# Kernel tuning notes

Hardware: AMD Instinct MI355X
Metric: run time of the kernel (lower is better)

## Reference

```python
import jax, jax.numpy as jnp
import numpy as np

DEGREES = (0, 1, 2, 3)
REPEATS = np.array([2 * l + 1 for l in DEGREES])          # [1,3,5,7]
EV_DIM = int(REPEATS.sum())                               # 16
SEG = np.concatenate([[0], np.cumsum(REPEATS)])
F, H, L = 128, 8, len(DEGREES)
DH, DE = F // H, F // L                                   # 16, 32
NRB, N, E = 32, 16384, 262144
ATT_NORM_INV = float(np.sqrt(DH))
ATT_NORM_EV = float(np.sqrt(DE))


def l0_contraction(ev):
    # per-degree sum of squares over the m components: [..., EV_DIM] -> [..., L]
    return jnp.stack([jnp.sum(ev[..., SEG[i]:SEG[i + 1]] ** 2, axis=-1) for i in range(L)], axis=-1)


def silu(x):
    return x * jax.nn.sigmoid(x)


def filter_net(rbf, ev_inv, w1r, b1r, w2r, b2r, w1e, b1e, w2e, b2e):
    # FilterNet(num_layers=2): Linear+SiLU then Linear+Identity on each branch, summed.
    r = silu(rbf @ w1r + b1r) @ w2r + b2r
    e = silu(ev_inv @ w1e + b1e) @ w2e + b2e
    return r + e


def setup_inputs() -> dict:
    key = jax.random.key(0)
    ks = iter(jax.random.split(key, 40))
    nrm = lambda shape, s=1.0: jax.random.normal(next(ks), shape, dtype=jnp.float32) * s
    s = 0.05
    inp = {
        'inv_features': nrm((N, F)),
        'ev_features': nrm((N, EV_DIM)),
        'rbf': jax.random.uniform(next(ks), (E, NRB), dtype=jnp.float32),
        'sh_vectors': nrm((E, EV_DIM)),
        'cutoffs': jax.random.uniform(next(ks), (E, 1), dtype=jnp.float32),
        'senders': jax.random.randint(next(ks), (E,), 0, N),
        'receivers': jax.random.randint(next(ks), (E,), 0, N),
    }
    for p in ('fi', 'fe'):
        inp[p + '_rbf_w1'] = nrm((NRB, F), s); inp[p + '_rbf_b1'] = jnp.zeros((F,), jnp.float32)
        inp[p + '_rbf_w2'] = nrm((F, F), s);   inp[p + '_rbf_b2'] = jnp.zeros((F,), jnp.float32)
        inp[p + '_ev_w1'] = nrm((L, F // 4), s); inp[p + '_ev_b1'] = jnp.zeros((F // 4,), jnp.float32)
        inp[p + '_ev_w2'] = nrm((F // 4, F), s); inp[p + '_ev_b2'] = jnp.zeros((F,), jnp.float32)
    inp['Wq_inv'] = nrm((H, DH, DH), s)
    inp['Wk_inv'] = nrm((H, DH, DH), s)
    inp['Wv_inv'] = nrm((H, DH, DH), s)
    inp['Wq_ev'] = nrm((L, DE, DE), s)
    inp['Wk_ev'] = nrm((L, DE, DE), s)
    inp['int_w'] = nrm((F + L, F + L), s)
    inp['int_b'] = jnp.zeros((F + L,), jnp.float32)
    return inp


def reference(inv_features, ev_features, rbf, sh_vectors, cutoffs,
              fi_rbf_w1, fi_rbf_b1, fi_rbf_w2, fi_rbf_b2, fi_ev_w1, fi_ev_b1, fi_ev_w2, fi_ev_b2,
              fe_rbf_w1, fe_rbf_b1, fe_rbf_w2, fe_rbf_b2, fe_ev_w1, fe_ev_b1, fe_ev_w2, fe_ev_b2,
              Wq_inv, Wk_inv, Wv_inv, Wq_ev, Wk_ev, int_w, int_b,
              senders, receivers):
    n_nodes = inv_features.shape[0]
    # --- EuclideanAttentionBlock ---
    ev_diff = ev_features[senders] - ev_features[receivers]           # [E, EV_DIM]
    ev_diff_inv = l0_contraction(ev_diff)                             # [E, L]
    fw_inv = filter_net(rbf, ev_diff_inv, fi_rbf_w1, fi_rbf_b1, fi_rbf_w2, fi_rbf_b2,
                        fi_ev_w1, fi_ev_b1, fi_ev_w2, fi_ev_b2).reshape(-1, H, DH)
    fw_ev = filter_net(rbf, ev_diff_inv, fe_rbf_w1, fe_rbf_b1, fe_rbf_w2, fe_rbf_b2,
                       fe_ev_w1, fe_ev_b1, fe_ev_w2, fe_ev_b2).reshape(-1, L, DE)
    x_inv = inv_features.reshape(-1, H, DH)
    x_ev = inv_features.reshape(-1, L, DE)
    # qk_non_linearity = identity (None default)
    q_inv = jnp.einsum('nhd,hde->nhe', x_inv, Wq_inv)[receivers]      # [E, H, DH]
    k_inv = jnp.einsum('nhd,hde->nhe', x_inv, Wk_inv)[senders]
    v_inv = jnp.einsum('nhd,hde->nhe', x_inv, Wv_inv)[senders]
    q_ev = jnp.einsum('nld,lde->nle', x_ev, Wq_ev)[receivers]         # [E, L, DE]
    k_ev = jnp.einsum('nld,lde->nle', x_ev, Wk_ev)[senders]
    alpha_inv = jnp.sum(q_inv * (k_inv * fw_inv), axis=-1, keepdims=True) / ATT_NORM_INV  # [E,H,1]
    alpha_ev = jnp.sum(q_ev * (k_ev * fw_ev), axis=-1) / ATT_NORM_EV                      # [E,L]
    scaled_inv = cutoffs[:, :, None] * alpha_inv * v_inv              # [E, H, DH]
    d_att_inv = jax.ops.segment_sum(scaled_inv, receivers, num_segments=n_nodes).reshape(-1, F)
    alpha_ev_full = jnp.repeat(alpha_ev, REPEATS, axis=-1, total_repeat_length=EV_DIM)    # [E, EV_DIM]
    scaled_ev = cutoffs * alpha_ev_full * sh_vectors
    d_att_ev = jax.ops.segment_sum(scaled_ev, receivers, num_segments=n_nodes)
    inv1 = inv_features + d_att_inv
    ev1 = ev_features + d_att_ev
    # --- InteractionBlock ---
    ev_inv = l0_contraction(ev1)                                      # [N, L]
    t = jnp.concatenate([inv1, ev_inv], axis=-1) @ int_w + int_b      # [N, F+L]
    d_inv2 = t[..., :F]
    b_ev = jnp.repeat(t[..., F:], REPEATS, axis=-1, total_repeat_length=EV_DIM)
    d_ev2 = b_ev * ev1
    return inv1 + d_inv2, ev1 + d_ev2
```

## Files before the change

### kernel.cpp

```cpp
#include <hip/hip_runtime.h>
#include <math.h>

#define NN 16384
#define NRB 32
#define EE 262144
#define TEB 64
#define TPB_E 16

typedef __attribute__((ext_vector_type(8))) short short8v;
typedef __attribute__((ext_vector_type(4))) float f32x4;

__device__ __forceinline__ float silu_f(float x) {
    return x * __builtin_amdgcn_rcpf(1.0f + __expf(-x));
}
__device__ __forceinline__ int degmap(int j) { return (j == 0) ? 0 : (j < 4) ? 1 : (j < 9) ? 2 : 3; }
__device__ __forceinline__ unsigned short f2b(float f) {
    unsigned int u = __float_as_uint(f);
    unsigned int r = (u + 0x7FFFu + ((u >> 16) & 1u)) >> 16;
    return (unsigned short)r;
}
__device__ __forceinline__ unsigned short f2bt(float f) {
    return (unsigned short)(__float_as_uint(f) >> 16);
}
__device__ __forceinline__ float b2f(short s) {
    return __uint_as_float(((unsigned int)(unsigned short)s) << 16);
}

__global__ __launch_bounds__(256) void fused_prep(
    const float* __restrict__ fi_w1r, const float* __restrict__ fi_w2r,
    const float* __restrict__ fi_w2e,
    const float* __restrict__ fe_w1r, const float* __restrict__ fe_w2r,
    const float* __restrict__ fe_w2e,
    unsigned short* __restrict__ wbf,
    const int* __restrict__ recv,
    int* __restrict__ cnt)
{
    const int tid = threadIdx.x;
    if (blockIdx.x < 192) {
        const int id = blockIdx.x * 256 + tid;
        if (id >= 2 * 24576) return;
        const int p = id / 24576;
        const int r = id % 24576;
        const float* w1r = p ? fe_w1r : fi_w1r;
        const float* w2r = p ? fe_w2r : fi_w2r;
        const float* w2e = p ? fe_w2e : fi_w2e;
        float v;
        if (r < 4096) {
            v = w1r[(r & 31) * 128 + (r >> 5)];
        } else if (r < 20480) {
            const int rr = r - 4096;
            v = w2r[(rr & 127) * 128 + (rr >> 7)];
        } else {
            const int rr = r - 20480;
            v = w2e[(rr & 31) * 128 + (rr >> 5)];
        }
        wbf[p * 24576 + r] = f2b(v);
    } else {
        const int e = (blockIdx.x - 192) * 256 + tid;
        if (e < EE) atomicAdd(&cnt[recv[e]], 1);
    }
}

__global__ __launch_bounds__(256) void csr_scan(const int* __restrict__ cnt,
                                                int* __restrict__ off) {
    __shared__ int ps[256];
    const int t = threadIdx.x;
    const int base = t * 64;
    int s = 0;
    for (int i = 0; i < 64; ++i) s += cnt[base + i];
    ps[t] = s;
    __syncthreads();
    for (int dd = 1; dd < 256; dd <<= 1) {
        int v = 0;
        if (t >= dd) v = ps[t - dd];
        __syncthreads();
        ps[t] += v;
        __syncthreads();
    }
    int run = ps[t] - s;
    for (int i = 0; i < 64; ++i) {
        off[base + i] = run;
        run += cnt[base + i];
    }
}

__global__ __launch_bounds__(256) void fused_fill(
    const int* __restrict__ recv,
    const int* __restrict__ send,
    const float* __restrict__ rbf,
    const float* __restrict__ cutoffs,
    const float* __restrict__ ev_feat,
    const float* __restrict__ sh,
    const int* __restrict__ off,
    int* __restrict__ cursor,
    int* __restrict__ s_sid,
    int* __restrict__ s_rid,
    unsigned short* __restrict__ rbf_s,
    float* __restrict__ cut_s,
    float* __restrict__ evinv_s,
    unsigned short* __restrict__ sh_s,
    const float* __restrict__ inv,
    const float* __restrict__ Wq_inv, const float* __restrict__ Wk_inv,
    const float* __restrict__ Wv_inv,
    const float* __restrict__ Wq_ev, const float* __restrict__ Wk_ev,
    unsigned short* __restrict__ q_inv, unsigned short* __restrict__ k_inv,
    unsigned short* __restrict__ v_inv,
    unsigned short* __restrict__ q_ev, unsigned short* __restrict__ k_ev)
{
    const int tid = threadIdx.x;
    if (blockIdx.x < 1024) {
        const int e = blockIdx.x * 256 + tid;
        if (e < EE) {
            const int r = recv[e];
            const int s = send[e];
            const int p = off[r] + atomicAdd(&cursor[r], 1);
            s_sid[p] = s;
            s_rid[p] = r;
            cut_s[p] = cutoffs[e];
            const float* src = rbf + (size_t)e * 32;
            unsigned short* dst = rbf_s + (size_t)p * 32;
            #pragma unroll
            for (int c = 0; c < 4; ++c) {
                const float4 a = *(const float4*)(src + c * 8);
                const float4 b = *(const float4*)(src + c * 8 + 4);
                short8v pk;
                pk[0] = f2b(a.x); pk[1] = f2b(a.y); pk[2] = f2b(a.z); pk[3] = f2b(a.w);
                pk[4] = f2b(b.x); pk[5] = f2b(b.y); pk[6] = f2b(b.z); pk[7] = f2b(b.w);
                *(short8v*)(dst + c * 8) = pk;
            }
            const float* shp = sh + (size_t)e * 16;
            unsigned short* shd = sh_s + (size_t)p * 16;
            #pragma unroll
            for (int c = 0; c < 2; ++c) {
                const float4 a = *(const float4*)(shp + c * 8);
                const float4 b = *(const float4*)(shp + c * 8 + 4);
                short8v pk;
                pk[0] = f2b(a.x); pk[1] = f2b(a.y); pk[2] = f2b(a.z); pk[3] = f2b(a.w);
                pk[4] = f2b(b.x); pk[5] = f2b(b.y); pk[6] = f2b(b.z); pk[7] = f2b(b.w);
                *(short8v*)(shd + c * 8) = pk;
            }
            const float* es = ev_feat + (size_t)s * 16;
            const float* er = ev_feat + (size_t)r * 16;
            float df[16];
            #pragma unroll
            for (int j = 0; j < 16; j += 4) {
                const float4 a = *(const float4*)(es + j);
                const float4 b = *(const float4*)(er + j);
                df[j] = a.x - b.x; df[j + 1] = a.y - b.y;
                df[j + 2] = a.z - b.z; df[j + 3] = a.w - b.w;
            }
            float4 ev4;
            ev4.x = df[0] * df[0];
            ev4.y = df[1] * df[1] + df[2] * df[2] + df[3] * df[3];
            float a2 = 0.f;
            #pragma unroll
            for (int j = 4; j < 9; ++j) a2 += df[j] * df[j];
            ev4.z = a2;
            float a3 = 0.f;
            #pragma unroll
            for (int j = 9; j < 16; ++j) a3 += df[j] * df[j];
            ev4.w = a3;
            *(float4*)(evinv_s + (size_t)p * 4) = ev4;
        }
    } else {
        const int b = blockIdx.x - 1024;
        const int t = tid & 127;
        const int half = tid >> 7;
        const int h = t >> 4, e = t & 15;
        const int l = t >> 5, e2 = t & 31;

        float wq[16], wk[16], wv[16];
        #pragma unroll
        for (int d = 0; d < 16; ++d) {
            wq[d] = Wq_inv[h * 256 + d * 16 + e];
            wk[d] = Wk_inv[h * 256 + d * 16 + e];
            wv[d] = Wv_inv[h * 256 + d * 16 + e];
        }
        float wqe[32], wke[32];
        #pragma unroll
        for (int d = 0; d < 32; ++d) {
            wqe[d] = Wq_ev[l * 1024 + d * 32 + e2];
            wke[d] = Wk_ev[l * 1024 + d * 32 + e2];
        }

        __shared__ float x[256];
        for (int nn = 0; nn < 4; ++nn) {
            const int n = b * 8 + nn * 2 + half;
            __syncthreads();
            x[half * 128 + t] = inv[(size_t)n * 128 + t];
            __syncthreads();
            float aq = 0.f, ak = 0.f, av = 0.f;
            #pragma unroll
            for (int d = 0; d < 16; ++d) {
                const float xv = x[half * 128 + h * 16 + d];
                aq += xv * wq[d]; ak += xv * wk[d]; av += xv * wv[d];
            }
            q_inv[(size_t)n * 128 + t] = f2b(aq);
            k_inv[(size_t)n * 128 + t] = f2b(ak);
            v_inv[(size_t)n * 128 + t] = f2b(av);
            float bq = 0.f, bk = 0.f;
            #pragma unroll
            for (int d = 0; d < 32; ++d) {
                const float xv = x[half * 128 + l * 32 + d];
                bq += xv * wqe[d]; bk += xv * wke[d];
            }
            q_ev[(size_t)n * 128 + t] = f2b(bq);
            k_ev[(size_t)n * 128 + t] = f2b(bk);
        }
    }
}

__global__ __launch_bounds__(256) void edge_kernel(
    const unsigned short* __restrict__ rbf_s,
    const float* __restrict__ cut_s,
    const float* __restrict__ evinv_s,
    const int* __restrict__ s_sid,
    const int* __restrict__ s_rid,
    const unsigned short* __restrict__ wbf,
    const float* __restrict__ fi_b1r, const float* __restrict__ fi_b2r,
    const float* __restrict__ fi_w1e, const float* __restrict__ fi_b1e,
    const float* __restrict__ fi_b2e,
    const float* __restrict__ fe_b1r, const float* __restrict__ fe_b2r,
    const float* __restrict__ fe_w1e, const float* __restrict__ fe_b1e,
    const float* __restrict__ fe_b2e,
    const unsigned short* __restrict__ q_inv, const unsigned short* __restrict__ k_inv,
    const unsigned short* __restrict__ q_ev, const unsigned short* __restrict__ k_ev,
    float* __restrict__ alpha_g)
{
    __shared__ unsigned short w2lds[16384];
    __shared__ unsigned short w1lds[4096];
    __shared__ unsigned short w2elds[4096];
    __shared__ unsigned short rbuf[TEB][40];
    __shared__ unsigned short h1buf[TEB][140];
    __shared__ unsigned short hebuf[TEB][40];
    __shared__ float evinv_t[TEB][4];

    const int tid = threadIdx.x;
    const int lane = tid & 63;
    const int wv = tid >> 6;
    const int wb = wv * 16;
    const int nchunk = gridDim.x >> 3;
    const int wgid = (blockIdx.x & 7) * nchunk + (blockIdx.x >> 3);
    const int e0 = wgid * (TEB * TPB_E);
    const int pass = blockIdx.y;
    const int lrow = lane & 15;
    const int lk = lane >> 4;
    const int rj = (lane & 3) * 8;
    const int rrow = lane >> 2;

    const float* b1r = pass ? fe_b1r : fi_b1r;
    const float* b2r = pass ? fe_b2r : fi_b2r;
    const float* w1e = pass ? fe_w1e : fi_w1e;
    const float* b1e = pass ? fe_b1e : fi_b1e;
    const float* b2e = pass ? fe_b2e : fi_b2e;
    const unsigned short* qtab = pass == 0 ? q_inv : q_ev;
    const unsigned short* ktab = pass == 0 ? k_inv : k_ev;

    {
        const short8v* src = (const short8v*)(wbf + pass * 24576 + 4096);
        short8v* dst = (short8v*)w2lds;
        #pragma unroll
        for (int i = 0; i < 8; ++i) {
            const int c = tid + 256 * i;
            const int col = c >> 4;
            const int slot = c & 15;
            dst[(c & ~15) | (slot ^ (col & 7))] = src[c];
        }
        const short8v* s1 = (const short8v*)(wbf + pass * 24576);
        const short8v* s2 = (const short8v*)(wbf + pass * 24576 + 20480);
        #pragma unroll
        for (int i = 0; i < 2; ++i) {
            const int c = tid + 256 * i;
            ((short8v*)w1lds)[(c & 3) * 128 + (c >> 2)] = s1[c];
            ((short8v*)w2elds)[(c & 3) * 128 + (c >> 2)] = s2[c];
        }
    }

    int sC, rC;
    float cC;
    short8v rbC;
    float4 evC;
    {
        const int ge = e0 + wb + lrow;
        sC = s_sid[ge]; rC = s_rid[ge]; cC = cut_s[ge];
        rbC = *(const short8v*)(rbf_s + (size_t)(e0 + wb + rrow) * 32 + rj);
        if (lane < 16)
            evC = *(const float4*)(evinv_s + (size_t)(e0 + wb + lane) * 4);
    }
    __syncthreads();

    #pragma unroll 1
    for (int t = 0; t < TPB_E; ++t) {
        const int tbase = e0 + t * TEB;

        const unsigned short* qb = qtab + (size_t)rC * 128 + lk * 32;
        const unsigned short* kb = ktab + (size_t)sC * 128 + lk * 32;
        const short8v pq0 = *(const short8v*)qb;
        const short8v pq1 = *(const short8v*)(qb + 8);
        const short8v pq2 = *(const short8v*)(qb + 16);
        const short8v pq3 = *(const short8v*)(qb + 24);
        const short8v pk0 = *(const short8v*)kb;
        const short8v pk1 = *(const short8v*)(kb + 8);
        const short8v pk2 = *(const short8v*)(kb + 16);
        const short8v pk3 = *(const short8v*)(kb + 24);

        int sN = 0, rN = 0;
        float cN = 0.f;
        short8v rbN;
        float4 evN;
        if (t + 1 < TPB_E) {
            const int gn = tbase + TEB + wb + lrow;
            sN = s_sid[gn]; rN = s_rid[gn]; cN = cut_s[gn];
            rbN = *(const short8v*)(rbf_s + (size_t)(tbase + TEB + wb + rrow) * 32 + rj);
            if (lane < 16)
                evN = *(const float4*)(evinv_s + (size_t)(tbase + TEB + wb + lane) * 4);
        }

        *(short8v*)&rbuf[wb + rrow][rj] = rbC;
        if (lane < 16)
            *(float4*)&evinv_t[wb + lane][0] = evC;

        {
            const short8v a1 = *(const short8v*)&rbuf[wb + lrow][lk * 8];
            #pragma unroll
            for (int tt = 0; tt < 8; ++tt) {
                const int col = tt * 16 + lrow;
                const float b = b1r[col];
                f32x4 c; c[0] = b; c[1] = b; c[2] = b; c[3] = b;
                const short8v bv = ((const short8v*)w1lds)[lk * 128 + col];
                c = __builtin_amdgcn_mfma_f32_16x16x32_bf16(a1, bv, c, 0, 0, 0);
                #pragma unroll
                for (int rg = 0; rg < 4; ++rg)
                    h1buf[wb + lk * 4 + rg][col] = f2bt(silu_f(c[rg]));
            }
        }
        {
            const int le = wb + rrow;
            const float v0 = evinv_t[le][0], v1 = evinv_t[le][1];
            const float v2 = evinv_t[le][2], v3 = evinv_t[le][3];
            short8v pk_;
            #pragma unroll
            for (int q = 0; q < 2; ++q) {
                const int j = rj + q * 4;
                const float4 bb = *(const float4*)(b1e + j);
                const float4 r0 = *(const float4*)(w1e + j);
                const float4 r1 = *(const float4*)(w1e + 32 + j);
                const float4 r2 = *(const float4*)(w1e + 64 + j);
                const float4 r3 = *(const float4*)(w1e + 96 + j);
                pk_[q * 4 + 0] = f2bt(silu_f(bb.x + v0 * r0.x + v1 * r1.x + v2 * r2.x + v3 * r3.x));
                pk_[q * 4 + 1] = f2bt(silu_f(bb.y + v0 * r0.y + v1 * r1.y + v2 * r2.y + v3 * r3.y));
                pk_[q * 4 + 2] = f2bt(silu_f(bb.z + v0 * r0.z + v1 * r1.z + v2 * r2.z + v3 * r3.z));
                pk_[q * 4 + 3] = f2bt(silu_f(bb.w + v0 * r0.w + v1 * r1.w + v2 * r2.w + v3 * r3.w));
            }
            *(short8v*)&hebuf[le][rj] = pk_;
        }

        f32x4 acc[8];
        #pragma unroll
        for (int tt = 0; tt < 8; ++tt) {
            const int col = tt * 16 + lrow;
            const float b = b2r[col] + b2e[col];
            acc[tt][0] = b; acc[tt][1] = b; acc[tt][2] = b; acc[tt][3] = b;
        }
        #pragma unroll
        for (int ks = 0; ks < 4; ++ks) {
            const short8v av = *(const short8v*)&h1buf[wb + lrow][ks * 32 + lk * 8];
            const int slot = ks * 4 + lk;
            #pragma unroll
            for (int tt = 0; tt < 8; ++tt) {
                const int col = tt * 16 + lrow;
                const short8v bv = *(const short8v*)&w2lds[
                    col * 128 + ((slot ^ (lrow & 7)) << 3)];
                acc[tt] = __builtin_amdgcn_mfma_f32_16x16x32_bf16(av, bv, acc[tt], 0, 0, 0);
            }
        }
        {
            const short8v ae = *(const short8v*)&hebuf[wb + lrow][lk * 8];
            #pragma unroll
            for (int tt = 0; tt < 8; ++tt) {
                const int col = tt * 16 + lrow;
                const short8v bv = ((const short8v*)w2elds)[lk * 128 + col];
                acc[tt] = __builtin_amdgcn_mfma_f32_16x16x32_bf16(ae, bv, acc[tt], 0, 0, 0);
            }
        }
        #pragma unroll
        for (int tt = 0; tt < 8; ++tt) {
            const int col = tt * 16 + lrow;
            #pragma unroll
            for (int rg = 0; rg < 4; ++rg)
                h1buf[wb + lk * 4 + rg][col] = f2bt(acc[tt][rg]);
        }

        const int slot = tbase + wb + lrow;
        if (pass == 0) {
            const int le = wb + lrow;
            #pragma unroll
            for (int it = 0; it < 2; ++it) {
                const int h = lk * 2 + it;
                const short8v f0 = *(const short8v*)&h1buf[le][h * 16];
                const short8v f1 = *(const short8v*)&h1buf[le][h * 16 + 8];
                const short8v qa = it ? pq2 : pq0;
                const short8v qc = it ? pq3 : pq1;
                const short8v ka = it ? pk2 : pk0;
                const short8v kc = it ? pk3 : pk1;
                float dot = 0.f;
                #pragma unroll
                for (int j = 0; j < 8; ++j)
                    dot += b2f(qa[j]) * b2f(ka[j]) * b2f(f0[j]);
                #pragma unroll
                for (int j = 0; j < 8; ++j)
                    dot += b2f(qc[j]) * b2f(kc[j]) * b2f(f1[j]);
                alpha_g[(size_t)slot * 12 + h] = dot * 0.25f * cC;
            }
        } else {
            const int le = wb + lrow;
            const int l = lk;
            float dot = 0.f;
            #pragma unroll
            for (int c8 = 0; c8 < 4; ++c8) {
                const short8v fv = *(const short8v*)&h1buf[le][l * 32 + c8 * 8];
                const short8v qv = (c8 == 0) ? pq0 : (c8 == 1) ? pq1 : (c8 == 2) ? pq2 : pq3;
                const short8v kv = (c8 == 0) ? pk0 : (c8 == 1) ? pk1 : (c8 == 2) ? pk2 : pk3;
                #pragma unroll
                for (int j = 0; j < 8; ++j)
                    dot += b2f(qv[j]) * b2f(kv[j]) * b2f(fv[j]);
            }
            alpha_g[(size_t)slot * 12 + 8 + l] = dot * 0.17677669529663687f * cC;
        }

        sC = sN; rC = rN; cC = cN; rbC = rbN; evC = evN;
    }
}

__global__ __launch_bounds__(256) void node_update(
    const float* __restrict__ inv, const float* __restrict__ ev,
    const unsigned short* __restrict__ v_inv,
    const unsigned short* __restrict__ sh_s,
    const float* __restrict__ alpha_g,
    const int* __restrict__ cnt, const int* __restrict__ off,
    const int* __restrict__ s_sid,
    const float* __restrict__ int_w, const float* __restrict__ int_b,
    float* __restrict__ out0, float* __restrict__ out1)
{
    const int tid = threadIdx.x;
    const int g16 = tid >> 4;
    const int fl16 = tid & 15;
    const int f16 = fl16 * 8;
    const int hsel = f16 >> 4;
    const int n = blockIdx.x;
    const int d = cnt[n];
    const int o = off[n];

    float accv[8];
    #pragma unroll
    for (int j = 0; j < 8; ++j) accv[j] = 0.f;
    float acce = 0.f;
    const int esel = 8 + degmap(fl16);

    for (int i = g16; i < d; i += 16) {
        const int p = o + i;
        const int sid = s_sid[p];
        const float a = alpha_g[(size_t)p * 12 + hsel];
        const short8v v = *(const short8v*)(v_inv + (size_t)sid * 128 + f16);
        #pragma unroll
        for (int j = 0; j < 8; ++j) accv[j] += a * b2f(v[j]);
        acce += alpha_g[(size_t)p * 12 + esel] * b2f(sh_s[(size_t)p * 16 + fl16]);
    }

    __shared__ float pv[16][128];
    __shared__ float pe[16][16];
    __shared__ float xin[132];
    __shared__ float ev1s[16];
    __shared__ float tcol[4];

    #pragma unroll
    for (int j = 0; j < 8; ++j) pv[g16][f16 + j] = accv[j];
    pe[g16][fl16] = acce;
    __syncthreads();

    float iv = 0.f;
    if (tid < 128) {
        float s = 0.f;
        #pragma unroll
        for (int gg = 0; gg < 16; ++gg) s += pv[gg][tid];
        iv = inv[(size_t)n * 128 + tid] + s;
        xin[tid] = iv;
        if (tid < 16) {
            float se = 0.f;
            #pragma unroll
            for (int gg = 0; gg < 16; ++gg) se += pe[gg][tid];
            ev1s[tid] = ev[(size_t)n * 16 + tid] + se;
        }
    }
    __syncthreads();
    if (tid < 4) {
        const int st = (tid == 0) ? 0 : (tid == 1) ? 1 : (tid == 2) ? 4 : 9;
        const int en = (tid == 0) ? 1 : (tid == 1) ? 4 : (tid == 2) ? 9 : 16;
        float a = 0.f;
        for (int j = st; j < en; ++j) a += ev1s[j] * ev1s[j];
        xin[128 + tid] = a;
    }
    __syncthreads();

    const int g = tid >> 5;
    const int fl = tid & 31;
    const int f = fl * 4;
    float4 macc; macc.x = 0.f; macc.y = 0.f; macc.z = 0.f; macc.w = 0.f;
    float macc2 = 0.f;
    const int k0 = g * 17;
    const int k1 = (k0 + 17 < 132) ? k0 + 17 : 132;
    for (int k = k0; k < k1; ++k) {
        const float xv = xin[k];
        const float4 w4 = *(const float4*)(int_w + k * 132 + f);
        macc.x += xv * w4.x; macc.y += xv * w4.y;
        macc.z += xv * w4.z; macc.w += xv * w4.w;
        if (fl < 4) macc2 += xv * int_w[k * 132 + 128 + fl];
    }
    __syncthreads();
    *reinterpret_cast<float4*>(&pv[g][f]) = macc;
    if (fl < 4) pe[g][fl] = macc2;
    __syncthreads();

    if (tid < 128) {
        float s = int_b[tid];
        #pragma unroll
        for (int gg = 0; gg < 8; ++gg) s += pv[gg][tid];
        out0[(size_t)n * 128 + tid] = iv + s;
        if (tid < 4) {
            float s2 = int_b[128 + tid];
            #pragma unroll
            for (int gg = 0; gg < 8; ++gg) s2 += pe[gg][tid];
            tcol[tid] = s2;
        }
    }
    __syncthreads();
    if (tid < 16) out1[(size_t)n * 16 + tid] = ev1s[tid] * (1.0f + tcol[degmap(tid)]);
}

extern "C" void kernel_launch(void* const* d_in, const int* in_sizes, int n_in,
                              void* d_out, int out_size, void* d_ws, size_t ws_size,
                              hipStream_t stream) {
    const float* inv_features = (const float*)d_in[0];
    const float* ev_features  = (const float*)d_in[1];
    const float* rbf          = (const float*)d_in[2];
    const float* sh_vectors   = (const float*)d_in[3];
    const float* cutoffs      = (const float*)d_in[4];
    const int*   senders      = (const int*)d_in[5];
    const int*   receivers    = (const int*)d_in[6];
    const float* fi_rbf_w1 = (const float*)d_in[7];
    const float* fi_rbf_b1 = (const float*)d_in[8];
    const float* fi_rbf_w2 = (const float*)d_in[9];
    const float* fi_rbf_b2 = (const float*)d_in[10];
    const float* fi_ev_w1  = (const float*)d_in[11];
    const float* fi_ev_b1  = (const float*)d_in[12];
    const float* fi_ev_w2  = (const float*)d_in[13];
    const float* fi_ev_b2  = (const float*)d_in[14];
    const float* fe_rbf_w1 = (const float*)d_in[15];
    const float* fe_rbf_b1 = (const float*)d_in[16];
    const float* fe_rbf_w2 = (const float*)d_in[17];
    const float* fe_rbf_b2 = (const float*)d_in[18];
    const float* fe_ev_w1  = (const float*)d_in[19];
    const float* fe_ev_b1  = (const float*)d_in[20];
    const float* fe_ev_w2  = (const float*)d_in[21];
    const float* fe_ev_b2  = (const float*)d_in[22];
    const float* Wq_inv = (const float*)d_in[23];
    const float* Wk_inv = (const float*)d_in[24];
    const float* Wv_inv = (const float*)d_in[25];
    const float* Wq_ev  = (const float*)d_in[26];
    const float* Wk_ev  = (const float*)d_in[27];
    const float* int_w  = (const float*)d_in[28];
    const float* int_b  = (const float*)d_in[29];

    float* ws = (float*)d_ws;
    unsigned short* q_inv = (unsigned short*)ws;
    unsigned short* k_inv = q_inv + (size_t)NN * 128;
    unsigned short* v_inv = q_inv + (size_t)NN * 256;
    unsigned short* q_ev  = q_inv + (size_t)NN * 384;
    unsigned short* k_ev  = q_inv + (size_t)NN * 512;
    float* alpha_g = ws + (size_t)NN * 320;
    int*   cnt     = (int*)(ws + (size_t)NN * 512);
    int*   off     = cnt + NN;
    int*   cursor  = cnt + 2 * NN;
    int*   s_sid   = cnt + 3 * NN;
    int*   s_rid   = s_sid + EE;
    float* cut_s   = (float*)(s_rid + EE);
    float* evinv_s = cut_s + EE;
    unsigned short* rbf_s = (unsigned short*)(evinv_s + (size_t)EE * 4);
    unsigned short* sh_s  = rbf_s + (size_t)EE * 32;
    unsigned short* wbf   = sh_s + (size_t)EE * 16;

    hipMemsetAsync(cnt, 0, (size_t)3 * NN * sizeof(int), stream);

    fused_prep<<<1216, 256, 0, stream>>>(fi_rbf_w1, fi_rbf_w2, fi_ev_w2,
                                         fe_rbf_w1, fe_rbf_w2, fe_ev_w2, wbf,
                                         receivers, cnt);

    csr_scan<<<1, 256, 0, stream>>>(cnt, off);

    fused_fill<<<3072, 256, 0, stream>>>(receivers, senders, rbf, cutoffs, ev_features,
                                         sh_vectors, off, cursor, s_sid, s_rid,
                                         rbf_s, cut_s, evinv_s, sh_s,
                                         inv_features, Wq_inv, Wk_inv, Wv_inv,
                                         Wq_ev, Wk_ev,
                                         q_inv, k_inv, v_inv, q_ev, k_ev);

    dim3 egrid(EE / (TEB * TPB_E), 2);
    edge_kernel<<<egrid, 256, 0, stream>>>(
        rbf_s, cut_s, evinv_s, s_sid, s_rid, wbf,
        fi_rbf_b1, fi_rbf_b2, fi_ev_w1, fi_ev_b1, fi_ev_b2,
        fe_rbf_b1, fe_rbf_b2, fe_ev_w1, fe_ev_b1, fe_ev_b2,
        q_inv, k_inv, q_ev, k_ev, alpha_g);

    node_update<<<NN, 256, 0, stream>>>(inv_features, ev_features, v_inv, sh_s,
                                        alpha_g, cnt, off, s_sid,
                                        int_w, int_b,
                                        (float*)d_out, (float*)d_out + (size_t)NN * 128);
}
```

Baseline: 240.2 us.

## Cut edge kernel LDS use: read small weights from global, permute via bpermute

Removes the w1, w2e, rbf, hebuf and evinv LDS staging buffers from the edge kernel. Small weight fragments are now loaded straight from global/L2 into registers each tile, rbf and evinv are loaded directly in MFMA operand layout, and the ev hidden activations are shuffled with ds_bpermute. A launch bound of 3 waves is added to target higher occupancy. This lowers LDS footprint and LDS traffic, at the cost of more global loads per tile and more register pressure.

```diff
diff --git a/kernel.cpp b/kernel.cpp
--- a/kernel.cpp
+++ b/kernel.cpp
@@ -210,7 +210,7 @@
     }
 }
 
-__global__ __launch_bounds__(256) void edge_kernel(
+__global__ __launch_bounds__(256, 3) void edge_kernel(
     const unsigned short* __restrict__ rbf_s,
     const float* __restrict__ cut_s,
     const float* __restrict__ evinv_s,
@@ -228,12 +228,7 @@
     float* __restrict__ alpha_g)
 {
     __shared__ unsigned short w2lds[16384];
-    __shared__ unsigned short w1lds[4096];
-    __shared__ unsigned short w2elds[4096];
-    __shared__ unsigned short rbuf[TEB][40];
     __shared__ unsigned short h1buf[TEB][140];
-    __shared__ unsigned short hebuf[TEB][40];
-    __shared__ float evinv_t[TEB][4];
 
     const int tid = threadIdx.x;
     const int lane = tid & 63;
@@ -255,6 +250,8 @@
     const float* b2e = pass ? fe_b2e : fi_b2e;
     const unsigned short* qtab = pass == 0 ? q_inv : q_ev;
     const unsigned short* ktab = pass == 0 ? k_inv : k_ev;
+    const unsigned short* w1g  = wbf + pass * 24576;
+    const unsigned short* w2eg = wbf + pass * 24576 + 20480;
 
     {
         const short8v* src = (const short8v*)(wbf + pass * 24576 + 4096);
@@ -265,14 +262,6 @@
             const int col = c >> 4;
             const int slot = c & 15;
             dst[(c & ~15) | (slot ^ (col & 7))] = src[c];
-        }
-        const short8v* s1 = (const short8v*)(wbf + pass * 24576);
-        const short8v* s2 = (const short8v*)(wbf + pass * 24576 + 20480);
-        #pragma unroll
-        for (int i = 0; i < 2; ++i) {
-            const int c = tid + 256 * i;
-            ((short8v*)w1lds)[(c & 3) * 128 + (c >> 2)] = s1[c];
-            ((short8v*)w2elds)[(c & 3) * 128 + (c >> 2)] = s2[c];
         }
     }
 
@@ -283,11 +272,12 @@
     {
         const int ge = e0 + wb + lrow;
         sC = s_sid[ge]; rC = s_rid[ge]; cC = cut_s[ge];
-        rbC = *(const short8v*)(rbf_s + (size_t)(e0 + wb + rrow) * 32 + rj);
-        if (lane < 16)
-            evC = *(const float4*)(evinv_s + (size_t)(e0 + wb + lane) * 4);
-    }
-    __syncthreads();
+        rbC = *(const short8v*)(rbf_s + (size_t)(e0 + wb + lrow) * 32 + lk * 8);
+        evC = *(const float4*)(evinv_s + (size_t)(e0 + wb + rrow) * 4);
+    }
+    __syncthreads();
+
+    const int baddr = (((lane & 15) << 2) | (lane >> 4)) << 2;
 
     #pragma unroll 1
     for (int t = 0; t < TPB_E; ++t) {
@@ -304,6 +294,11 @@
         const short8v pk2 = *(const short8v*)(kb + 16);
         const short8v pk3 = *(const short8v*)(kb + 24);
 
+        short8v w1f[8];
+        #pragma unroll
+        for (int tt = 0; tt < 8; ++tt)
+            w1f[tt] = *(const short8v*)(w1g + (tt * 16 + lrow) * 32 + lk * 8);
+
         int sN = 0, rN = 0;
         float cN = 0.f;
         short8v rbN;
@@ -311,33 +306,26 @@
         if (t + 1 < TPB_E) {
             const int gn = tbase + TEB + wb + lrow;
             sN = s_sid[gn]; rN = s_rid[gn]; cN = cut_s[gn];
-            rbN = *(const short8v*)(rbf_s + (size_t)(tbase + TEB + wb + rrow) * 32 + rj);
-            if (lane < 16)
-                evN = *(const float4*)(evinv_s + (size_t)(tbase + TEB + wb + lane) * 4);
-        }
-
-        *(short8v*)&rbuf[wb + rrow][rj] = rbC;
-        if (lane < 16)
-            *(float4*)&evinv_t[wb + lane][0] = evC;
+            rbN = *(const short8v*)(rbf_s + (size_t)(tbase + TEB + wb + lrow) * 32 + lk * 8);
+            evN = *(const float4*)(evinv_s + (size_t)(tbase + TEB + wb + rrow) * 4);
+        }
 
         {
-            const short8v a1 = *(const short8v*)&rbuf[wb + lrow][lk * 8];
+            const short8v a1 = rbC;
             #pragma unroll
             for (int tt = 0; tt < 8; ++tt) {
                 const int col = tt * 16 + lrow;
                 const float b = b1r[col];
                 f32x4 c; c[0] = b; c[1] = b; c[2] = b; c[3] = b;
-                const short8v bv = ((const short8v*)w1lds)[lk * 128 + col];
-                c = __builtin_amdgcn_mfma_f32_16x16x32_bf16(a1, bv, c, 0, 0, 0);
+                c = __builtin_amdgcn_mfma_f32_16x16x32_bf16(a1, w1f[tt], c, 0, 0, 0);
                 #pragma unroll
                 for (int rg = 0; rg < 4; ++rg)
                     h1buf[wb + lk * 4 + rg][col] = f2bt(silu_f(c[rg]));
             }
         }
+        short8v ae;
         {
-            const int le = wb + rrow;
-            const float v0 = evinv_t[le][0], v1 = evinv_t[le][1];
-            const float v2 = evinv_t[le][2], v3 = evinv_t[le][3];
+            const float v0 = evC.x, v1 = evC.y, v2 = evC.z, v3 = evC.w;
             short8v pk_;
             #pragma unroll
             for (int q = 0; q < 2; ++q) {
@@ -352,8 +340,19 @@
                 pk_[q * 4 + 2] = f2bt(silu_f(bb.z + v0 * r0.z + v1 * r1.z + v2 * r2.z + v3 * r3.z));
                 pk_[q * 4 + 3] = f2bt(silu_f(bb.w + v0 * r0.w + v1 * r1.w + v2 * r2.w + v3 * r3.w));
             }
-            *(short8v*)&hebuf[le][rj] = pk_;
-        }
+            union { short8v v; int i[4]; } u; u.v = pk_;
+            union { int i[4]; short8v v; } o;
+            o.i[0] = __builtin_amdgcn_ds_bpermute(baddr, u.i[0]);
+            o.i[1] = __builtin_amdgcn_ds_bpermute(baddr, u.i[1]);
+            o.i[2] = __builtin_amdgcn_ds_bpermute(baddr, u.i[2]);
+            o.i[3] = __builtin_amdgcn_ds_bpermute(baddr, u.i[3]);
+            ae = o.v;
+        }
+
+        short8v w2ef[8];
+        #pragma unroll
+        for (int tt = 0; tt < 8; ++tt)
+            w2ef[tt] = *(const short8v*)(w2eg + (tt * 16 + lrow) * 32 + lk * 8);
 
         f32x4 acc[8];
         #pragma unroll
@@ -374,15 +373,10 @@
                 acc[tt] = __builtin_amdgcn_mfma_f32_16x16x32_bf16(av, bv, acc[tt], 0, 0, 0);
             }
         }
-        {
-            const short8v ae = *(const short8v*)&hebuf[wb + lrow][lk * 8];
-            #pragma unroll
-            for (int tt = 0; tt < 8; ++tt) {
-                const int col = tt * 16 + lrow;
-                const short8v bv = ((const short8v*)w2elds)[lk * 128 + col];
-                acc[tt] = __builtin_amdgcn_mfma_f32_16x16x32_bf16(ae, bv, acc[tt], 0, 0, 0);
-            }
-        }
+        #pragma unroll
+        for (int tt = 0; tt < 8; ++tt)
+            acc[tt] = __builtin_amdgcn_mfma_f32_16x16x32_bf16(ae, w2ef[tt], acc[tt], 0, 0, 0);
+
         #pragma unroll
         for (int tt = 0; tt < 8; ++tt) {
             const int col = tt * 16 + lrow;
```

New measurement: 403.1 us. +67.8%, slower.
